# Optimization experiments

Measured on AMD Instinct MI355X. Metric: run time of the kernel, lower is better.

Reference implementation:

```python
import jax, jax.numpy as jnp
import numpy as np

N_NODES = 100000
N_EDGES = 1600000
D_IN = 128
D_OUT = 128


def setup_inputs() -> dict:
    key = jax.random.key(0)
    k1, k2, k3, k4, k5 = jax.random.split(key, 5)
    h = jax.random.normal(k1, (N_NODES, D_IN), dtype=jnp.float32)
    src = jax.random.randint(k2, (N_EDGES,), 0, N_NODES, dtype=jnp.int64)
    dst = jax.random.randint(k3, (N_EDGES,), 0, N_NODES, dtype=jnp.int64)
    W = jax.random.normal(k4, (2 * D_IN, D_OUT), dtype=jnp.float32) * (1.0 / np.sqrt(2 * D_IN))
    b = jax.random.normal(k5, (D_OUT,), dtype=jnp.float32) * 0.01
    return {"h": h, "src": src, "dst": dst, "W": W, "b": b}


def reference(h, src, dst, W, b):
    # copy_u + mean: scatter-mean of source features onto destination nodes
    msg_sum = jax.ops.segment_sum(h[src], dst, num_segments=N_NODES)  # [N, D_IN]
    deg = jax.ops.segment_sum(jnp.ones((src.shape[0],), h.dtype), dst, num_segments=N_NODES)  # [N]
    h_N = jnp.where(deg[:, None] > 0, msg_sum / jnp.maximum(deg, 1.0)[:, None], 0.0)
    h_total = jnp.concatenate([h, h_N], axis=1)  # [N, 2*D_IN]
    return h_total @ W + b
```

## Files before the change

### kernel.cpp

```cpp
#include <hip/hip_runtime.h>
#include <stdint.h>

#define N_NODES 100000
#define D 128
#define BN 128
#define NB ((N_NODES + BN - 1) / BN)
#define EPB 8192
#define CAP 2816

typedef short bf16x8 __attribute__((ext_vector_type(8)));
typedef float f32x4 __attribute__((ext_vector_type(4)));

__device__ __forceinline__ float bf2f(unsigned short u) {
    return __uint_as_float(((unsigned int)u) << 16);
}
__device__ __forceinline__ unsigned short f2bf(float f) {
    unsigned int x = __float_as_uint(f);
    unsigned int r = x + 0x7fffu + ((x >> 16) & 1u);
    return (unsigned short)(r >> 16);
}

__global__ __launch_bounds__(256) void prep_k(
    const float* __restrict__ h, unsigned short* __restrict__ h_bf,
    const float* __restrict__ W, unsigned short* __restrict__ Wf,
    const int* __restrict__ src, const int* __restrict__ dst,
    int* __restrict__ cnt, unsigned int* __restrict__ pairs,
    int n_edges, int part_blocks)
{
    __shared__ int hist[NB];
    __shared__ int gbase[NB];
    __shared__ int lc[NB];

    int bid = blockIdx.x;
    int t = threadIdx.x;

    if (bid < part_blocks) {
        for (int i = t; i < NB; i += 256) { hist[i] = 0; lc[i] = 0; }
        __syncthreads();
        int base = bid * EPB;
        int lim = n_edges - base; if (lim > EPB) lim = EPB;
        for (int i = t; i < lim; i += 256)
            atomicAdd(&hist[dst[base + i] >> 7], 1);
        __syncthreads();
        for (int i = t; i < NB; i += 256) {
            int c = hist[i];
            gbase[i] = c ? atomicAdd(&cnt[i], c) : 0;
        }
        __syncthreads();
        for (int i = t; i < lim; i += 256) {
            int e = base + i;
            int d = dst[e], b = d >> 7;
            int slot = atomicAdd(&lc[b], 1);
            int off = gbase[b] + slot;
            if (off < CAP)
                pairs[(size_t)b * CAP + off] =
                    (unsigned int)src[e] | ((unsigned int)(d & 127) << 17);
        }
    } else if (bid < part_blocks + 16) {
        int gid = (bid - part_blocks) * 256 + t;
        if (gid < 64 * 64) {
            int f = gid >> 6, l = gid & 63;
            int kt = f >> 3, ct = f & 7;
            int n = ct * 16 + (l & 15);
            int kb = kt * 32 + (l >> 4) * 8;
            #pragma unroll
            for (int j = 0; j < 8; ++j)
                Wf[(size_t)f * 512 + l * 8 + j] = f2bf(W[(size_t)(kb + j) * D + n]);
        }
    } else {
        size_t base = ((size_t)(bid - part_blocks - 16) * 256 + t) * 4;
        if (base < (size_t)N_NODES * D) {
            float4 v = *(const float4*)(h + base);
            ushort4 o;
            o.x = f2bf(v.x); o.y = f2bf(v.y); o.z = f2bf(v.z); o.w = f2bf(v.w);
            *(ushort4*)(h_bf + base) = o;
        }
    }
}

__global__ __launch_bounds__(512, 8) void agg3_k(
    const unsigned short* __restrict__ h_bf, const unsigned int* __restrict__ pairs,
    const int* __restrict__ cnt_g, unsigned short* __restrict__ hN_bf)
{
    __shared__ unsigned int lp[CAP];
    __shared__ unsigned int srt[CAP];
    __shared__ int counts[BN];
    __shared__ int startp[BN];
    __shared__ int cursor[BN];

    int t = threadIdx.x;
    int b = blockIdx.x;
    size_t e0 = (size_t)b * CAP;
    int cnt = cnt_g[b];
    if (cnt > CAP) cnt = CAP;

    if (t < BN) counts[t] = 0;
    __syncthreads();

    for (int i = t; i < cnt; i += 512) {
        unsigned int p = pairs[e0 + i];
        lp[i] = p;
        atomicAdd(&counts[p >> 17], 1);
    }
    __syncthreads();

    if (t < BN) startp[t] = counts[t];
    __syncthreads();
    #pragma unroll
    for (int off = 1; off < BN; off <<= 1) {
        int v = 0;
        if (t < BN && t >= off) v = startp[t - off];
        __syncthreads();
        if (t < BN) startp[t] += v;
        __syncthreads();
    }
    if (t < BN) {
        int ex = startp[t] - counts[t];
        startp[t] = ex;
        cursor[t] = ex;
    }
    __syncthreads();

    for (int i = t; i < cnt; i += 512) {
        unsigned int p = lp[i];
        int s = atomicAdd(&cursor[p >> 17], 1);
        srt[s] = p & 0x1FFFFu;
    }
    __syncthreads();

    int wv = t >> 6, l = t & 63;
    int nbase = b * BN;
    for (int nl = wv; nl < BN; nl += 8) {
        int n = nbase + nl;
        if (n >= N_NODES) break;
        int dg = counts[nl], s0 = startp[nl];
        float ax = 0.f, ay = 0.f;
        int e = 0;
        for (; e + 4 <= dg; e += 4) {
            int i0 = srt[s0 + e],     i1 = srt[s0 + e + 1];
            int i2 = srt[s0 + e + 2], i3 = srt[s0 + e + 3];
            unsigned int u0 = *(const unsigned int*)(h_bf + (size_t)i0 * D + l * 2);
            unsigned int u1 = *(const unsigned int*)(h_bf + (size_t)i1 * D + l * 2);
            unsigned int u2 = *(const unsigned int*)(h_bf + (size_t)i2 * D + l * 2);
            unsigned int u3 = *(const unsigned int*)(h_bf + (size_t)i3 * D + l * 2);
            ax += (bf2f(u0 & 0xffff) + bf2f(u1 & 0xffff)) + (bf2f(u2 & 0xffff) + bf2f(u3 & 0xffff));
            ay += (bf2f(u0 >> 16) + bf2f(u1 >> 16)) + (bf2f(u2 >> 16) + bf2f(u3 >> 16));
        }
        for (; e < dg; ++e) {
            int i0 = srt[s0 + e];
            unsigned int u = *(const unsigned int*)(h_bf + (size_t)i0 * D + l * 2);
            ax += bf2f(u & 0xffff); ay += bf2f(u >> 16);
        }
        float invd = dg > 0 ? 1.0f / (float)dg : 0.f;
        unsigned int o = ((unsigned int)f2bf(ay * invd) << 16) | f2bf(ax * invd);
        *(unsigned int*)(hN_bf + (size_t)n * D + l * 2) = o;
    }
}

__global__ __launch_bounds__(256) void gemm_k(
    const unsigned short* __restrict__ h_bf, const unsigned short* __restrict__ hN_bf,
    const unsigned short* __restrict__ Wf, const float* __restrict__ bias,
    float* __restrict__ out)
{
    int tid = threadIdx.x;
    int w = tid >> 6, l = tid & 63;
    int n0 = blockIdx.x * 128 + w * 32;
    int lrow = l & 15, lq = l >> 4;

    int r0 = n0 + lrow;      if (r0 > N_NODES - 1) r0 = N_NODES - 1;
    int r1 = n0 + 16 + lrow; if (r1 > N_NODES - 1) r1 = N_NODES - 1;

    f32x4 acc[2][8];
    #pragma unroll
    for (int rg = 0; rg < 2; ++rg)
        #pragma unroll
        for (int ct = 0; ct < 8; ++ct)
            acc[rg][ct] = (f32x4){0.f, 0.f, 0.f, 0.f};

    const unsigned short* wf_lane = Wf + l * 8;

    #pragma unroll
    for (int kt = 0; kt < 8; ++kt) {
        const unsigned short* Abase = (kt < 4) ? h_bf : hN_bf;
        int ko = (kt & 3) * 32 + lq * 8;
        bf16x8 a0 = *(const bf16x8*)(Abase + (size_t)r0 * D + ko);
        bf16x8 a1 = *(const bf16x8*)(Abase + (size_t)r1 * D + ko);
        #pragma unroll
        for (int ct = 0; ct < 8; ++ct) {
            bf16x8 bfr = *(const bf16x8*)(wf_lane + (size_t)(kt * 8 + ct) * 512);
            acc[0][ct] = __builtin_amdgcn_mfma_f32_16x16x32_bf16(a0, bfr, acc[0][ct], 0, 0, 0);
            acc[1][ct] = __builtin_amdgcn_mfma_f32_16x16x32_bf16(a1, bfr, acc[1][ct], 0, 0, 0);
        }
    }

    int col = l & 15, q = l >> 4;
    #pragma unroll
    for (int ct = 0; ct < 8; ++ct) {
        float bv = bias[ct * 16 + col];
        #pragma unroll
        for (int rg = 0; rg < 2; ++rg) {
            #pragma unroll
            for (int r = 0; r < 4; ++r) {
                int row = n0 + rg * 16 + q * 4 + r;
                if (row < N_NODES)
                    out[(size_t)row * D + ct * 16 + col] = acc[rg][ct][r] + bv;
            }
        }
    }
}


extern "C" void kernel_launch(void* const* d_in, const int* in_sizes, int n_in,
                              void* d_out, int out_size, void* d_ws, size_t ws_size,
                              hipStream_t stream) {
    const float* h  = (const float*)d_in[0];
    const int* src  = (const int*)d_in[1];
    const int* dst  = (const int*)d_in[2];
    const float* W  = (const float*)d_in[3];
    const float* b  = (const float*)d_in[4];
    float* out      = (float*)d_out;
    int n_edges = in_sizes[1];

    char* ws = (char*)d_ws;
    unsigned short* h_bf  = (unsigned short*)ws;
    unsigned short* hN_bf = h_bf + (size_t)N_NODES * D;
    unsigned int* pairs   = (unsigned int*)(hN_bf + (size_t)N_NODES * D);
    unsigned short* Wf    = (unsigned short*)(pairs + (size_t)NB * CAP);
    int* cnt              = (int*)(Wf + 64 * 512);

    hipMemsetAsync(cnt, 0, NB * sizeof(int), stream);

    int pb = (n_edges + EPB - 1) / EPB;
    int cblocks = (int)(((size_t)N_NODES * D / 4 + 255) / 256);
    hipLaunchKernelGGL(prep_k, dim3(pb + 16 + cblocks), dim3(256), 0, stream,
                       h, h_bf, W, Wf, src, dst, cnt, pairs, n_edges, pb);

    hipLaunchKernelGGL(agg3_k, dim3(NB), dim3(512), 0, stream,
                       h_bf, pairs, cnt, hN_bf);
    hipLaunchKernelGGL(gemm_k, dim3((N_NODES + 127) / 128), dim3(256), 0, stream,
                       h_bf, hN_bf, Wf, b, out);
}
```

Before: 257.8 us.

## Halve aggregation bucket size and gather two edges per wave with 8-byte loads

Buckets now cover 64 destination nodes instead of 128, with the per-bucket capacity shrunk to match. This doubles the number of aggregation blocks and cuts shared memory per block. Inside the aggregation, each wave splits into two half-waves that each process a different edge, with lanes loading 4 bf16 values (8 bytes) at a time. The two partial sums are combined with a cross-half shuffle before the write. The aim is more loads in flight and more parallelism for the gather. The risks are bucket overflow at the smaller capacity, and a masked single-edge tail step that wastes half the wave.

```diff
diff --git a/kernel.cpp b/kernel.cpp
--- a/kernel.cpp
+++ b/kernel.cpp
@@ -3,10 +3,10 @@
 
 #define N_NODES 100000
 #define D 128
-#define BN 128
+#define BN 64
 #define NB ((N_NODES + BN - 1) / BN)
 #define EPB 8192
-#define CAP 2816
+#define CAP 1536
 
 typedef short bf16x8 __attribute__((ext_vector_type(8)));
 typedef float f32x4 __attribute__((ext_vector_type(4)));
@@ -40,7 +40,7 @@
         int base = bid * EPB;
         int lim = n_edges - base; if (lim > EPB) lim = EPB;
         for (int i = t; i < lim; i += 256)
-            atomicAdd(&hist[dst[base + i] >> 7], 1);
+            atomicAdd(&hist[dst[base + i] >> 6], 1);
         __syncthreads();
         for (int i = t; i < NB; i += 256) {
             int c = hist[i];
@@ -49,12 +49,12 @@
         __syncthreads();
         for (int i = t; i < lim; i += 256) {
             int e = base + i;
-            int d = dst[e], b = d >> 7;
+            int d = dst[e], b = d >> 6;
             int slot = atomicAdd(&lc[b], 1);
             int off = gbase[b] + slot;
             if (off < CAP)
                 pairs[(size_t)b * CAP + off] =
-                    (unsigned int)src[e] | ((unsigned int)(d & 127) << 17);
+                    (unsigned int)src[e] | ((unsigned int)(d & 63) << 17);
         }
     } else if (bid < part_blocks + 16) {
         int gid = (bid - part_blocks) * 256 + t;
@@ -129,31 +129,60 @@
     __syncthreads();
 
     int wv = t >> 6, l = t & 63;
+    int half = l >> 5, j = l & 31;
     int nbase = b * BN;
     for (int nl = wv; nl < BN; nl += 8) {
         int n = nbase + nl;
         if (n >= N_NODES) break;
         int dg = counts[nl], s0 = startp[nl];
-        float ax = 0.f, ay = 0.f;
+        float a0 = 0.f, a1 = 0.f, a2 = 0.f, a3 = 0.f;
         int e = 0;
-        for (; e + 4 <= dg; e += 4) {
-            int i0 = srt[s0 + e],     i1 = srt[s0 + e + 1];
-            int i2 = srt[s0 + e + 2], i3 = srt[s0 + e + 3];
-            unsigned int u0 = *(const unsigned int*)(h_bf + (size_t)i0 * D + l * 2);
-            unsigned int u1 = *(const unsigned int*)(h_bf + (size_t)i1 * D + l * 2);
-            unsigned int u2 = *(const unsigned int*)(h_bf + (size_t)i2 * D + l * 2);
-            unsigned int u3 = *(const unsigned int*)(h_bf + (size_t)i3 * D + l * 2);
-            ax += (bf2f(u0 & 0xffff) + bf2f(u1 & 0xffff)) + (bf2f(u2 & 0xffff) + bf2f(u3 & 0xffff));
-            ay += (bf2f(u0 >> 16) + bf2f(u1 >> 16)) + (bf2f(u2 >> 16) + bf2f(u3 >> 16));
-        }
-        for (; e < dg; ++e) {
-            int i0 = srt[s0 + e];
-            unsigned int u = *(const unsigned int*)(h_bf + (size_t)i0 * D + l * 2);
-            ax += bf2f(u & 0xffff); ay += bf2f(u >> 16);
-        }
+        for (; e + 8 <= dg; e += 8) {
+            int r0 = srt[s0 + e     + half];
+            int r1 = srt[s0 + e + 2 + half];
+            int r2 = srt[s0 + e + 4 + half];
+            int r3 = srt[s0 + e + 6 + half];
+            uint2 u0 = *(const uint2*)(h_bf + (size_t)r0 * D + j * 4);
+            uint2 u1 = *(const uint2*)(h_bf + (size_t)r1 * D + j * 4);
+            uint2 u2 = *(const uint2*)(h_bf + (size_t)r2 * D + j * 4);
+            uint2 u3 = *(const uint2*)(h_bf + (size_t)r3 * D + j * 4);
+            a0 += (__uint_as_float(u0.x << 16) + __uint_as_float(u1.x << 16))
+                + (__uint_as_float(u2.x << 16) + __uint_as_float(u3.x << 16));
+            a1 += (__uint_as_float(u0.x & 0xffff0000u) + __uint_as_float(u1.x & 0xffff0000u))
+                + (__uint_as_float(u2.x & 0xffff0000u) + __uint_as_float(u3.x & 0xffff0000u));
+            a2 += (__uint_as_float(u0.y << 16) + __uint_as_float(u1.y << 16))
+                + (__uint_as_float(u2.y << 16) + __uint_as_float(u3.y << 16));
+            a3 += (__uint_as_float(u0.y & 0xffff0000u) + __uint_as_float(u1.y & 0xffff0000u))
+                + (__uint_as_float(u2.y & 0xffff0000u) + __uint_as_float(u3.y & 0xffff0000u));
+        }
+        for (; e + 2 <= dg; e += 2) {
+            int r = srt[s0 + e + half];
+            uint2 u = *(const uint2*)(h_bf + (size_t)r * D + j * 4);
+            a0 += __uint_as_float(u.x << 16);
+            a1 += __uint_as_float(u.x & 0xffff0000u);
+            a2 += __uint_as_float(u.y << 16);
+            a3 += __uint_as_float(u.y & 0xffff0000u);
+        }
+        if (e < dg) {
+            int r = srt[s0 + e];
+            uint2 u = *(const uint2*)(h_bf + (size_t)r * D + j * 4);
+            float m = half ? 0.f : 1.f;
+            a0 += m * __uint_as_float(u.x << 16);
+            a1 += m * __uint_as_float(u.x & 0xffff0000u);
+            a2 += m * __uint_as_float(u.y << 16);
+            a3 += m * __uint_as_float(u.y & 0xffff0000u);
+        }
+        a0 += __shfl_xor(a0, 32);
+        a1 += __shfl_xor(a1, 32);
+        a2 += __shfl_xor(a2, 32);
+        a3 += __shfl_xor(a3, 32);
         float invd = dg > 0 ? 1.0f / (float)dg : 0.f;
-        unsigned int o = ((unsigned int)f2bf(ay * invd) << 16) | f2bf(ax * invd);
-        *(unsigned int*)(hN_bf + (size_t)n * D + l * 2) = o;
+        if (half == 0) {
+            uint2 o;
+            o.x = ((unsigned int)f2bf(a1 * invd) << 16) | f2bf(a0 * invd);
+            o.y = ((unsigned int)f2bf(a3 * invd) << 16) | f2bf(a2 * invd);
+            *(uint2*)(hN_bf + (size_t)n * D + j * 4) = o;
+        }
     }
 }
 
```

New measurement: 261.3 us. No clear change (+1.4%).
